# Kernel optimization log

Measured on AMD Instinct MI355X. Metric: run time of the kernel, lower is better.

Reference implementation:

```python
import jax, jax.numpy as jnp
import numpy as np


def _hilbert_d2xy(n, d):
    # standard Hilbert curve: distance d -> (x, y) on n x n grid (n power of 2)
    x = y = 0
    t = d
    s = 1
    while s < n:
        rx = 1 & (t // 2)
        ry = 1 & (t ^ rx)
        if ry == 0:
            if rx == 1:
                x = s - 1 - x
                y = s - 1 - y
            x, y = y, x
        x += s * rx
        y += s * ry
        t //= 4
        s *= 2
    return x, y


def _hilbert_perm(seq_len):
    n = int(round(np.sqrt(seq_len)))
    assert n * n == seq_len
    perm = np.empty(seq_len, dtype=np.int32)
    for d in range(seq_len):
        x, y = _hilbert_d2xy(n, d)
        perm[d] = y * n + x  # linear (row-major) index visited at Hilbert step d
    return perm


def setup_inputs() -> dict:
    key = jax.random.key(0)
    k1, k2, k3 = jax.random.split(key, 3)
    B, S, H, D = 1, 4096, 8, 64
    q = jax.random.normal(k1, (B, S, H, D), dtype=jnp.float32)
    k = jax.random.normal(k2, (B, S, H, D), dtype=jnp.float32)
    v = jax.random.normal(k3, (B, S, H, D), dtype=jnp.float32)
    hilbert_perm = jnp.asarray(_hilbert_perm(S))
    return {"q": q, "k": k, "v": v, "hilbert_perm": hilbert_perm}


def reference(q, k, v, hilbert_perm):
    B, S, H, D = q.shape
    inv_perm = jnp.argsort(hilbert_perm)

    # apply_hilbert_ordering along dim=1 (seq): gather by permutation
    q_o = q[:, hilbert_perm]
    k_o = k[:, hilbert_perm]
    v_o = v[:, hilbert_perm]

    # faithful to original: raw flat reshape of [B,S,H,D] -> [B*H, S, D]
    q_f = q_o.reshape(B * H, S, D)
    k_f = k_o.reshape(B * H, S, D)
    v_f = v_o.reshape(B * H, S, D)

    scale = 1.0 / jnp.sqrt(jnp.asarray(D, dtype=q.dtype))
    scores = jnp.einsum('bsd,btd->bst', q_f, k_f) * scale  # [B*H, S, S]
    attn = jax.nn.softmax(scores, axis=-1)
    out_f = jnp.einsum('bst,btd->bsd', attn, v_f)  # [B*H, S, D]

    out = out_f.reshape(B, H, S, D).transpose(0, 2, 1, 3).reshape(B, S, H, D)
    # inverse Hilbert ordering along dim=1
    return out[:, inv_perm]
```

## Files before the change

### kernel.cpp

```cpp
#include <hip/hip_runtime.h>

typedef _Float16 f16;
typedef _Float16 f16x4 __attribute__((ext_vector_type(4)));
typedef _Float16 f16x8 __attribute__((ext_vector_type(8)));
typedef __fp16 fp16x2 __attribute__((ext_vector_type(2)));
typedef float f32x4 __attribute__((ext_vector_type(4)));

#define MFMA_16x16x32_F16(A, B, C) __builtin_amdgcn_mfma_f32_16x16x32_f16((A), (B), (C), 0, 0, 0)

typedef const __attribute__((address_space(1))) char gchar;
typedef __attribute__((address_space(3))) char lchar;

__device__ __forceinline__ float fexp2(float x) { return __builtin_amdgcn_exp2f(x); }
__device__ __forceinline__ int swzb(int b) { return b ^ ((b >> 3) & 0x70); }

namespace {
constexpr int SB = 4096;
constexpr size_t BB = (size_t)SB * 64 * 2;
}

__device__ __forceinline__ int kinv(int r) {
    return 32 * (r >> 5) + 8 * ((r >> 2) & 3) + 4 * ((r >> 4) & 1) + (r & 3);
}

__global__ __launch_bounds__(256)
void hilbert_prepass_kernel(const float* __restrict__ kp, const float* __restrict__ vp,
                            const int* __restrict__ perm,
                            char* __restrict__ kw, char* __restrict__ vtw)
{
    const int bid = blockIdx.x;
    const int batch = bid & 7;
    const int tile = bid >> 3;
    const int tid = (int)threadIdx.x;
    const int r = tid >> 2;
    const int c4 = tid & 3;

    __shared__ float Vl[64][68];

    const int t = tile * 64 + r;
    const int srow = perm[batch * 512 + (t >> 3)];
    const size_t boff = (size_t)srow * 512 + (t & 7) * 64 + c4 * 16;

    {
        const float* ks = kp + boff;
        const float4 k0 = *(const float4*)(ks + 0);
        const float4 k1 = *(const float4*)(ks + 4);
        const float4 k2 = *(const float4*)(ks + 8);
        const float4 k3 = *(const float4*)(ks + 12);
        f16x8 h0, h1;
        h0[0] = (f16)k0.x; h0[1] = (f16)k0.y; h0[2] = (f16)k0.z; h0[3] = (f16)k0.w;
        h0[4] = (f16)k1.x; h0[5] = (f16)k1.y; h0[6] = (f16)k1.z; h0[7] = (f16)k1.w;
        h1[0] = (f16)k2.x; h1[1] = (f16)k2.y; h1[2] = (f16)k2.z; h1[3] = (f16)k2.w;
        h1[4] = (f16)k3.x; h1[5] = (f16)k3.y; h1[6] = (f16)k3.z; h1[7] = (f16)k3.w;
        char* kt = kw + (size_t)batch * BB + (size_t)tile * 8192;
        const int o = r * 128 + c4 * 32;
        *(f16x8*)(kt + swzb(o)) = h0;
        *(f16x8*)(kt + swzb(o + 16)) = h1;
    }
    {
        const float* vs = vp + boff;
        *(float4*)&Vl[r][c4 * 16 + 0]  = *(const float4*)(vs + 0);
        *(float4*)&Vl[r][c4 * 16 + 4]  = *(const float4*)(vs + 4);
        *(float4*)&Vl[r][c4 * 16 + 8]  = *(const float4*)(vs + 8);
        *(float4*)&Vl[r][c4 * 16 + 12] = *(const float4*)(vs + 12);
    }
    __syncthreads();
    {
        const int d = tid >> 2;
        const int a = tid & 3;
        char* vt = vtw + (size_t)batch * BB + (size_t)tile * 8192;
        const int b0 = 32 * (a >> 1) + 4 * (a & 1);
#pragma unroll
        for (int gp = 0; gp < 4; ++gp) {
            f16x4 qv;
#pragma unroll
            for (int v = 0; v < 4; ++v) qv[v] = (f16)Vl[16 * a + 4 * gp + v][d];
            *(f16x4*)(vt + swzb(d * 128 + (b0 + 8 * gp) * 2)) = qv;
        }
    }
}

__global__ __launch_bounds__(512, 2)
void hilbert_attn_kernel(const float* __restrict__ qp,
                         const int* __restrict__ perm,
                         const char* __restrict__ kw, const char* __restrict__ vtw,
                         float* __restrict__ op)
{
    __shared__ __align__(16) char SM[65536];

    const int bid = blockIdx.x;
    const int batch = bid & 7;
    const int qbase = (bid >> 3) * 128;
    const int tid = (int)threadIdx.x;
    const int w = tid >> 6;
    const int lane = tid & 63;
    const int l16 = lane & 15;
    const int g = lane >> 4;
    const int half = w >> 2;
    const int wq = w & 3;
    const int swz = (l16 & 7) << 4;

    f16x8 Qf0[2], Qf1[2];
    {
        constexpr float qscl = 0.125f * 1.44269504088896340736f;
#pragma unroll
        for (int s = 0; s < 2; ++s) {
            const int t = qbase + wq * 32 + s * 16 + l16;
            const int srow = perm[batch * 512 + (t >> 3)];
            const float* src = qp + (size_t)srow * 512 + (t & 7) * 64 + g * 8;
#pragma unroll
            for (int kt = 0; kt < 2; ++kt) {
                const float4 x0 = *(const float4*)(src + 32 * kt);
                const float4 x1 = *(const float4*)(src + 32 * kt + 4);
                f16x8 f;
                f[0] = (f16)(x0.x * qscl); f[1] = (f16)(x0.y * qscl);
                f[2] = (f16)(x0.z * qscl); f[3] = (f16)(x0.w * qscl);
                f[4] = (f16)(x1.x * qscl); f[5] = (f16)(x1.y * qscl);
                f[6] = (f16)(x1.z * qscl); f[7] = (f16)(x1.w * qscl);
                if (s == 0) Qf0[kt] = f; else Qf1[kt] = f;
            }
        }
    }

    f32x4 oacc0[4], oacc1[4];
#pragma unroll
    for (int i = 0; i < 4; ++i) {
        oacc0[i] = (f32x4){0.f, 0.f, 0.f, 0.f};
        oacc1[i] = (f32x4){0.f, 0.f, 0.f, 0.f};
    }
    float lr0 = 0.f, lr1 = 0.f;

    const char* ksrc = kw + (size_t)batch * BB + (size_t)tid * 16;
    const char* vsrc = vtw + (size_t)batch * BB + (size_t)tid * 16;

    union U8 { f16x8 v; fp16x2 h[4]; };

    {
        lchar* dst = (lchar*)&SM[w << 10];
        __builtin_amdgcn_global_load_lds((gchar*)(ksrc), dst, 16, 0, 0);
        __builtin_amdgcn_global_load_lds((gchar*)(ksrc + 8192), dst + 8192, 16, 0, 0);
        __builtin_amdgcn_global_load_lds((gchar*)(vsrc), dst + 16384, 16, 0, 0);
        __builtin_amdgcn_global_load_lds((gchar*)(vsrc + 8192), dst + 24576, 16, 0, 0);
    }
    asm volatile("s_waitcnt vmcnt(0)" ::: "memory");
    __builtin_amdgcn_s_barrier();

    for (int it = 0; it < 31; ++it) {
        const int cur = it & 1;
        const int kbb = cur * 32768 + half * 8192;
        const int vbb = cur * 32768 + 16384 + half * 8192;
        const size_t go = (size_t)(it + 1) * 16384;
        lchar* dstb = (lchar*)&SM[(cur ^ 1) * 32768 + (w << 10)];

        __builtin_amdgcn_global_load_lds((gchar*)(ksrc + go), dstb, 16, 0, 0);
        __builtin_amdgcn_global_load_lds((gchar*)(ksrc + go + 8192), dstb + 8192, 16, 0, 0);

        f32x4 sa0[4], sa1[4];
#pragma unroll
        for (int i = 0; i < 4; ++i) {
            sa0[i] = (f32x4){0.f, 0.f, 0.f, 0.f};
            sa1[i] = (f32x4){0.f, 0.f, 0.f, 0.f};
        }
        __builtin_amdgcn_s_setprio(1);
#pragma unroll
        for (int kt = 0; kt < 2; ++kt) {
#pragma unroll
            for (int mt = 0; mt < 4; ++mt) {
                const int off = kbb + (l16 + 16 * mt) * 128 + (((g + 4 * kt) * 16) ^ swz);
                const f16x8 kf = *(const f16x8*)&SM[off];
                sa0[mt] = MFMA_16x16x32_F16(kf, Qf0[kt], sa0[mt]);
                sa1[mt] = MFMA_16x16x32_F16(kf, Qf1[kt], sa1[mt]);
            }
        }
        __builtin_amdgcn_s_setprio(0);

        __builtin_amdgcn_global_load_lds((gchar*)(vsrc + go), dstb + 16384, 16, 0, 0);
        __builtin_amdgcn_global_load_lds((gchar*)(vsrc + go + 8192), dstb + 24576, 16, 0, 0);

        U8 p0k0, p0k1, p1k0, p1k1;
#pragma unroll
        for (int mt = 0; mt < 4; ++mt) {
            const float a0 = fexp2(sa0[mt][0]);
            const float a1 = fexp2(sa0[mt][1]);
            const float a2 = fexp2(sa0[mt][2]);
            const float a3 = fexp2(sa0[mt][3]);
            lr0 += (a0 + a1) + (a2 + a3);
            const float b0 = fexp2(sa1[mt][0]);
            const float b1 = fexp2(sa1[mt][1]);
            const float b2 = fexp2(sa1[mt][2]);
            const float b3 = fexp2(sa1[mt][3]);
            lr1 += (b0 + b1) + (b2 + b3);
            if (mt < 2) {
                p0k0.h[2 * mt]     = __builtin_amdgcn_cvt_pkrtz(a0, a1);
                p0k0.h[2 * mt + 1] = __builtin_amdgcn_cvt_pkrtz(a2, a3);
                p1k0.h[2 * mt]     = __builtin_amdgcn_cvt_pkrtz(b0, b1);
                p1k0.h[2 * mt + 1] = __builtin_amdgcn_cvt_pkrtz(b2, b3);
            } else {
                p0k1.h[2 * (mt - 2)]     = __builtin_amdgcn_cvt_pkrtz(a0, a1);
                p0k1.h[2 * (mt - 2) + 1] = __builtin_amdgcn_cvt_pkrtz(a2, a3);
                p1k1.h[2 * (mt - 2)]     = __builtin_amdgcn_cvt_pkrtz(b0, b1);
                p1k1.h[2 * (mt - 2) + 1] = __builtin_amdgcn_cvt_pkrtz(b2, b3);
            }
        }

        asm volatile("s_waitcnt vmcnt(4)" ::: "memory");
        __builtin_amdgcn_s_barrier();

        __builtin_amdgcn_s_setprio(1);
#pragma unroll
        for (int kt = 0; kt < 2; ++kt) {
            const f16x8 pf0 = kt ? p0k1.v : p0k0.v;
            const f16x8 pf1 = kt ? p1k1.v : p1k0.v;
#pragma unroll
            for (int mtd = 0; mtd < 4; ++mtd) {
                const int voff = vbb + (l16 + 16 * mtd) * 128 + (((g + 4 * kt) * 16) ^ swz);
                const f16x8 vf = *(const f16x8*)&SM[voff];
                oacc0[mtd] = MFMA_16x16x32_F16(vf, pf0, oacc0[mtd]);
                oacc1[mtd] = MFMA_16x16x32_F16(vf, pf1, oacc1[mtd]);
            }
        }
        __builtin_amdgcn_s_setprio(0);

        asm volatile("s_waitcnt vmcnt(2)" ::: "memory");
        __builtin_amdgcn_s_barrier();
    }

    {
        const int kbb = 32768 + half * 8192;
        const int vbb = 32768 + 16384 + half * 8192;

        f32x4 sa0[4], sa1[4];
#pragma unroll
        for (int i = 0; i < 4; ++i) {
            sa0[i] = (f32x4){0.f, 0.f, 0.f, 0.f};
            sa1[i] = (f32x4){0.f, 0.f, 0.f, 0.f};
        }
#pragma unroll
        for (int kt = 0; kt < 2; ++kt) {
#pragma unroll
            for (int mt = 0; mt < 4; ++mt) {
                const int off = kbb + (l16 + 16 * mt) * 128 + (((g + 4 * kt) * 16) ^ swz);
                const f16x8 kf = *(const f16x8*)&SM[off];
                sa0[mt] = MFMA_16x16x32_F16(kf, Qf0[kt], sa0[mt]);
                sa1[mt] = MFMA_16x16x32_F16(kf, Qf1[kt], sa1[mt]);
            }
        }
        U8 p0k0, p0k1, p1k0, p1k1;
#pragma unroll
        for (int mt = 0; mt < 4; ++mt) {
            const float a0 = fexp2(sa0[mt][0]);
            const float a1 = fexp2(sa0[mt][1]);
            const float a2 = fexp2(sa0[mt][2]);
            const float a3 = fexp2(sa0[mt][3]);
            lr0 += (a0 + a1) + (a2 + a3);
            const float b0 = fexp2(sa1[mt][0]);
            const float b1 = fexp2(sa1[mt][1]);
            const float b2 = fexp2(sa1[mt][2]);
            const float b3 = fexp2(sa1[mt][3]);
            lr1 += (b0 + b1) + (b2 + b3);
            if (mt < 2) {
                p0k0.h[2 * mt]     = __builtin_amdgcn_cvt_pkrtz(a0, a1);
                p0k0.h[2 * mt + 1] = __builtin_amdgcn_cvt_pkrtz(a2, a3);
                p1k0.h[2 * mt]     = __builtin_amdgcn_cvt_pkrtz(b0, b1);
                p1k0.h[2 * mt + 1] = __builtin_amdgcn_cvt_pkrtz(b2, b3);
            } else {
                p0k1.h[2 * (mt - 2)]     = __builtin_amdgcn_cvt_pkrtz(a0, a1);
                p0k1.h[2 * (mt - 2) + 1] = __builtin_amdgcn_cvt_pkrtz(a2, a3);
                p1k1.h[2 * (mt - 2)]     = __builtin_amdgcn_cvt_pkrtz(b0, b1);
                p1k1.h[2 * (mt - 2) + 1] = __builtin_amdgcn_cvt_pkrtz(b2, b3);
            }
        }
        asm volatile("s_waitcnt vmcnt(0)" ::: "memory");
        __builtin_amdgcn_s_barrier();
#pragma unroll
        for (int kt = 0; kt < 2; ++kt) {
            const f16x8 pf0 = kt ? p0k1.v : p0k0.v;
            const f16x8 pf1 = kt ? p1k1.v : p1k0.v;
#pragma unroll
            for (int mtd = 0; mtd < 4; ++mtd) {
                const int voff = vbb + (l16 + 16 * mtd) * 128 + (((g + 4 * kt) * 16) ^ swz);
                const f16x8 vf = *(const f16x8*)&SM[voff];
                oacc0[mtd] = MFMA_16x16x32_F16(vf, pf0, oacc0[mtd]);
                oacc1[mtd] = MFMA_16x16x32_F16(vf, pf1, oacc1[mtd]);
            }
        }
    }

    lr0 += __shfl_xor(lr0, 16);
    lr0 += __shfl_xor(lr0, 32);
    lr1 += __shfl_xor(lr1, 16);
    lr1 += __shfl_xor(lr1, 32);

    __syncthreads();

    float* OB = (float*)SM;
    float* ML = (float*)&SM[32768];
    if (w >= 4) {
        float* ob = OB + wq * 2048;
#pragma unroll
        for (int mtd = 0; mtd < 4; ++mtd) {
            *(f32x4*)&ob[l16 * 64 + mtd * 16 + g * 4] = oacc0[mtd];
            *(f32x4*)&ob[(16 + l16) * 64 + mtd * 16 + g * 4] = oacc1[mtd];
        }
        if (g == 0) {
            ML[wq * 32 + l16] = lr0;
            ML[wq * 32 + 16 + l16] = lr1;
        }
    }
    __syncthreads();
    if (w < 4) {
        float* ob = OB + wq * 2048;
#pragma unroll
        for (int s = 0; s < 2; ++s) {
            const float lmine = (s == 0) ? lr0 : lr1;
            const float linv = 1.f / (lmine + ML[wq * 32 + s * 16 + l16]);
            const int t = qbase + wq * 32 + s * 16 + l16;
            const int srow = perm[t];
            float* dst = op + (size_t)srow * 512 + batch * 64 + 4 * g;
#pragma unroll
            for (int mtd = 0; mtd < 4; ++mtd) {
                const f32x4 mine = (s == 0) ? oacc0[mtd] : oacc1[mtd];
                const f32x4 o2 = *(const f32x4*)&ob[(s * 16 + l16) * 64 + mtd * 16 + g * 4];
                float4 o;
                o.x = (mine[0] + o2[0]) * linv;
                o.y = (mine[1] + o2[1]) * linv;
                o.z = (mine[2] + o2[2]) * linv;
                o.w = (mine[3] + o2[3]) * linv;
                *(float4*)(dst + 16 * mtd) = o;
            }
        }
    }
}

extern "C" void kernel_launch(void* const* d_in, const int* in_sizes, int n_in,
                              void* d_out, int out_size, void* d_ws, size_t ws_size,
                              hipStream_t stream) {
    (void)in_sizes; (void)n_in; (void)out_size; (void)ws_size;
    const float* q = (const float*)d_in[0];
    const float* k = (const float*)d_in[1];
    const float* v = (const float*)d_in[2];
    const int* perm = (const int*)d_in[3];
    float* out = (float*)d_out;
    char* kw = (char*)d_ws;
    char* vtw = kw + 8 * BB;
    hipLaunchKernelGGL(hilbert_prepass_kernel, dim3(512), dim3(256), 0, stream,
                       k, v, perm, kw, vtw);
    hipLaunchKernelGGL(hilbert_attn_kernel, dim3(256), dim3(512), 0, stream,
                       q, perm, kw, vtw, out);
}
```

Before: 50.54 us.

## Software-pipeline QK^T of next tile with softmax and PV of current tile

```diff
diff --git a/kernel.cpp b/kernel.cpp
--- a/kernel.cpp
+++ b/kernel.cpp
@@ -135,60 +135,92 @@
 
     union U8 { f16x8 v; fp16x2 h[4]; };
 
-    {
-        lchar* dst = (lchar*)&SM[w << 10];
-        __builtin_amdgcn_global_load_lds((gchar*)(ksrc), dst, 16, 0, 0);
-        __builtin_amdgcn_global_load_lds((gchar*)(ksrc + 8192), dst + 8192, 16, 0, 0);
-        __builtin_amdgcn_global_load_lds((gchar*)(vsrc), dst + 16384, 16, 0, 0);
-        __builtin_amdgcn_global_load_lds((gchar*)(vsrc + 8192), dst + 24576, 16, 0, 0);
-    }
-    asm volatile("s_waitcnt vmcnt(0)" ::: "memory");
+#define STAGE_K(dstbuf, p)                                                           \
+    do {                                                                             \
+        lchar* d_ = (lchar*)&SM[(dstbuf) * 32768 + (w << 10)];                       \
+        const char* s_ = ksrc + (size_t)(p) * 16384;                                 \
+        __builtin_amdgcn_global_load_lds((gchar*)(s_), d_, 16, 0, 0);                \
+        __builtin_amdgcn_global_load_lds((gchar*)(s_ + 8192), d_ + 8192, 16, 0, 0);  \
+    } while (0)
+#define STAGE_V(dstbuf, p)                                                           \
+    do {                                                                             \
+        lchar* d_ = (lchar*)&SM[(dstbuf) * 32768 + 16384 + (w << 10)];               \
+        const char* s_ = vsrc + (size_t)(p) * 16384;                                 \
+        __builtin_amdgcn_global_load_lds((gchar*)(s_), d_, 16, 0, 0);                \
+        __builtin_amdgcn_global_load_lds((gchar*)(s_ + 8192), d_ + 8192, 16, 0, 0);  \
+    } while (0)
+
+    STAGE_K(0, 0);
+    STAGE_V(0, 0);
+    STAGE_K(1, 1);
+    asm volatile("s_waitcnt vmcnt(2)" ::: "memory");
     __builtin_amdgcn_s_barrier();
 
-    for (int it = 0; it < 31; ++it) {
-        const int cur = it & 1;
-        const int kbb = cur * 32768 + half * 8192;
-        const int vbb = cur * 32768 + 16384 + half * 8192;
-        const size_t go = (size_t)(it + 1) * 16384;
-        lchar* dstb = (lchar*)&SM[(cur ^ 1) * 32768 + (w << 10)];
-
-        __builtin_amdgcn_global_load_lds((gchar*)(ksrc + go), dstb, 16, 0, 0);
-        __builtin_amdgcn_global_load_lds((gchar*)(ksrc + go + 8192), dstb + 8192, 16, 0, 0);
-
-        f32x4 sa0[4], sa1[4];
-#pragma unroll
-        for (int i = 0; i < 4; ++i) {
-            sa0[i] = (f32x4){0.f, 0.f, 0.f, 0.f};
-            sa1[i] = (f32x4){0.f, 0.f, 0.f, 0.f};
-        }
-        __builtin_amdgcn_s_setprio(1);
+    f32x4 sp0[4], sp1[4];
+#pragma unroll
+    for (int i = 0; i < 4; ++i) {
+        sp0[i] = (f32x4){0.f, 0.f, 0.f, 0.f};
+        sp1[i] = (f32x4){0.f, 0.f, 0.f, 0.f};
+    }
+    {
+        const int kbb = half * 8192;
 #pragma unroll
         for (int kt = 0; kt < 2; ++kt) {
 #pragma unroll
             for (int mt = 0; mt < 4; ++mt) {
                 const int off = kbb + (l16 + 16 * mt) * 128 + (((g + 4 * kt) * 16) ^ swz);
                 const f16x8 kf = *(const f16x8*)&SM[off];
-                sa0[mt] = MFMA_16x16x32_F16(kf, Qf0[kt], sa0[mt]);
-                sa1[mt] = MFMA_16x16x32_F16(kf, Qf1[kt], sa1[mt]);
-            }
-        }
-        __builtin_amdgcn_s_setprio(0);
-
-        __builtin_amdgcn_global_load_lds((gchar*)(vsrc + go), dstb + 16384, 16, 0, 0);
-        __builtin_amdgcn_global_load_lds((gchar*)(vsrc + go + 8192), dstb + 24576, 16, 0, 0);
+                sp0[mt] = MFMA_16x16x32_F16(kf, Qf0[kt], sp0[mt]);
+                sp1[mt] = MFMA_16x16x32_F16(kf, Qf1[kt], sp1[mt]);
+            }
+        }
+    }
+    __builtin_amdgcn_s_barrier();
+    STAGE_V(1, 1);
+
+    for (int n = 0; n < 31; ++n) {
+        const int cur = n & 1, nxt = cur ^ 1;
+        const int p2 = (n + 2 > 31) ? 31 : n + 2;
+
+        STAGE_K(cur, p2);
+
+        asm volatile("s_waitcnt vmcnt(4)" ::: "memory");
+        __builtin_amdgcn_s_barrier();
+
+        f32x4 sn0[4], sn1[4];
+#pragma unroll
+        for (int i = 0; i < 4; ++i) {
+            sn0[i] = (f32x4){0.f, 0.f, 0.f, 0.f};
+            sn1[i] = (f32x4){0.f, 0.f, 0.f, 0.f};
+        }
+        {
+            const int kbb = nxt * 32768 + half * 8192;
+            __builtin_amdgcn_s_setprio(1);
+#pragma unroll
+            for (int kt = 0; kt < 2; ++kt) {
+#pragma unroll
+                for (int mt = 0; mt < 4; ++mt) {
+                    const int off = kbb + (l16 + 16 * mt) * 128 + (((g + 4 * kt) * 16) ^ swz);
+                    const f16x8 kf = *(const f16x8*)&SM[off];
+                    sn0[mt] = MFMA_16x16x32_F16(kf, Qf0[kt], sn0[mt]);
+                    sn1[mt] = MFMA_16x16x32_F16(kf, Qf1[kt], sn1[mt]);
+                }
+            }
+            __builtin_amdgcn_s_setprio(0);
+        }
 
         U8 p0k0, p0k1, p1k0, p1k1;
 #pragma unroll
         for (int mt = 0; mt < 4; ++mt) {
-            const float a0 = fexp2(sa0[mt][0]);
-            const float a1 = fexp2(sa0[mt][1]);
-            const float a2 = fexp2(sa0[mt][2]);
-            const float a3 = fexp2(sa0[mt][3]);
+            const float a0 = fexp2(sp0[mt][0]);
+            const float a1 = fexp2(sp0[mt][1]);
+            const float a2 = fexp2(sp0[mt][2]);
+            const float a3 = fexp2(sp0[mt][3]);
             lr0 += (a0 + a1) + (a2 + a3);
-            const float b0 = fexp2(sa1[mt][0]);
-            const float b1 = fexp2(sa1[mt][1]);
-            const float b2 = fexp2(sa1[mt][2]);
-            const float b3 = fexp2(sa1[mt][3]);
+            const float b0 = fexp2(sp1[mt][0]);
+            const float b1 = fexp2(sp1[mt][1]);
+            const float b2 = fexp2(sp1[mt][2]);
+            const float b3 = fexp2(sp1[mt][3]);
             lr1 += (b0 + b1) + (b2 + b3);
             if (mt < 2) {
                 p0k0.h[2 * mt]     = __builtin_amdgcn_cvt_pkrtz(a0, a1);
@@ -203,60 +235,46 @@
             }
         }
 
-        asm volatile("s_waitcnt vmcnt(4)" ::: "memory");
+        {
+            const int vbb = cur * 32768 + 16384 + half * 8192;
+            __builtin_amdgcn_s_setprio(1);
+#pragma unroll
+            for (int kt = 0; kt < 2; ++kt) {
+                const f16x8 pf0 = kt ? p0k1.v : p0k0.v;
+                const f16x8 pf1 = kt ? p1k1.v : p1k0.v;
+#pragma unroll
+                for (int mtd = 0; mtd < 4; ++mtd) {
+                    const int voff = vbb + (l16 + 16 * mtd) * 128 + (((g + 4 * kt) * 16) ^ swz);
+                    const f16x8 vf = *(const f16x8*)&SM[voff];
+                    oacc0[mtd] = MFMA_16x16x32_F16(vf, pf0, oacc0[mtd]);
+                    oacc1[mtd] = MFMA_16x16x32_F16(vf, pf1, oacc1[mtd]);
+                }
+            }
+            __builtin_amdgcn_s_setprio(0);
+        }
+
         __builtin_amdgcn_s_barrier();
-
-        __builtin_amdgcn_s_setprio(1);
-#pragma unroll
-        for (int kt = 0; kt < 2; ++kt) {
-            const f16x8 pf0 = kt ? p0k1.v : p0k0.v;
-            const f16x8 pf1 = kt ? p1k1.v : p1k0.v;
-#pragma unroll
-            for (int mtd = 0; mtd < 4; ++mtd) {
-                const int voff = vbb + (l16 + 16 * mtd) * 128 + (((g + 4 * kt) * 16) ^ swz);
-                const f16x8 vf = *(const f16x8*)&SM[voff];
-                oacc0[mtd] = MFMA_16x16x32_F16(vf, pf0, oacc0[mtd]);
-                oacc1[mtd] = MFMA_16x16x32_F16(vf, pf1, oacc1[mtd]);
-            }
-        }
-        __builtin_amdgcn_s_setprio(0);
-
-        asm volatile("s_waitcnt vmcnt(2)" ::: "memory");
-        __builtin_amdgcn_s_barrier();
-    }
-
-    {
-        const int kbb = 32768 + half * 8192;
-        const int vbb = 32768 + 16384 + half * 8192;
-
-        f32x4 sa0[4], sa1[4];
-#pragma unroll
-        for (int i = 0; i < 4; ++i) {
-            sa0[i] = (f32x4){0.f, 0.f, 0.f, 0.f};
-            sa1[i] = (f32x4){0.f, 0.f, 0.f, 0.f};
-        }
-#pragma unroll
-        for (int kt = 0; kt < 2; ++kt) {
-#pragma unroll
-            for (int mt = 0; mt < 4; ++mt) {
-                const int off = kbb + (l16 + 16 * mt) * 128 + (((g + 4 * kt) * 16) ^ swz);
-                const f16x8 kf = *(const f16x8*)&SM[off];
-                sa0[mt] = MFMA_16x16x32_F16(kf, Qf0[kt], sa0[mt]);
-                sa1[mt] = MFMA_16x16x32_F16(kf, Qf1[kt], sa1[mt]);
-            }
-        }
+        STAGE_V(cur, p2);
+
+#pragma unroll
+        for (int i = 0; i < 4; ++i) { sp0[i] = sn0[i]; sp1[i] = sn1[i]; }
+    }
+
+    asm volatile("s_waitcnt vmcnt(0)" ::: "memory");
+    __builtin_amdgcn_s_barrier();
+    {
         U8 p0k0, p0k1, p1k0, p1k1;
 #pragma unroll
         for (int mt = 0; mt < 4; ++mt) {
-            const float a0 = fexp2(sa0[mt][0]);
-            const float a1 = fexp2(sa0[mt][1]);
-            const float a2 = fexp2(sa0[mt][2]);
-            const float a3 = fexp2(sa0[mt][3]);
+            const float a0 = fexp2(sp0[mt][0]);
+            const float a1 = fexp2(sp0[mt][1]);
+            const float a2 = fexp2(sp0[mt][2]);
+            const float a3 = fexp2(sp0[mt][3]);
             lr0 += (a0 + a1) + (a2 + a3);
-            const float b0 = fexp2(sa1[mt][0]);
-            const float b1 = fexp2(sa1[mt][1]);
-            const float b2 = fexp2(sa1[mt][2]);
-            const float b3 = fexp2(sa1[mt][3]);
+            const float b0 = fexp2(sp1[mt][0]);
+            const float b1 = fexp2(sp1[mt][1]);
+            const float b2 = fexp2(sp1[mt][2]);
+            const float b3 = fexp2(sp1[mt][3]);
             lr1 += (b0 + b1) + (b2 + b3);
             if (mt < 2) {
                 p0k0.h[2 * mt]     = __builtin_amdgcn_cvt_pkrtz(a0, a1);
@@ -270,8 +288,7 @@
                 p1k1.h[2 * (mt - 2) + 1] = __builtin_amdgcn_cvt_pkrtz(b2, b3);
             }
         }
-        asm volatile("s_waitcnt vmcnt(0)" ::: "memory");
-        __builtin_amdgcn_s_barrier();
+        const int vbb = 32768 + 16384 + half * 8192;
 #pragma unroll
         for (int kt = 0; kt < 2; ++kt) {
             const f16x8 pf0 = kt ? p0k1.v : p0k0.v;
@@ -285,6 +302,8 @@
             }
         }
     }
+#undef STAGE_K
+#undef STAGE_V
 
     lr0 += __shfl_xor(lr0, 16);
     lr0 += __shfl_xor(lr0, 32);
```

Result: slower. 52.50 us (+3.9%).
